# Kernel optimization log

Hardware: AMD Instinct MI355X
Metric: run time of the kernel (lower is better)

The kernel has to match this reference:

```python
import jax, jax.numpy as jnp
import numpy as np

N_HEAD = 16
N_EMBD = 1024
BLOCK = 2048
B, T = 4, 2048


def setup_inputs() -> dict:
    key = jax.random.key(0)
    ks = jax.random.split(key, 5)
    scale = 1.0 / np.sqrt(N_EMBD)
    return {
        "x": jax.random.normal(ks[0], (B, T, N_EMBD), dtype=jnp.float32),
        "W_attn": jax.random.normal(ks[1], (N_EMBD, 3 * N_EMBD), dtype=jnp.float32) * scale,
        "b_attn": jax.random.normal(ks[2], (3 * N_EMBD,), dtype=jnp.float32) * 0.02,
        "W_proj": jax.random.normal(ks[3], (N_EMBD, N_EMBD), dtype=jnp.float32) * scale,
        "b_proj": jax.random.normal(ks[4], (N_EMBD,), dtype=jnp.float32) * 0.02,
    }


def reference(x, W_attn, b_attn, W_proj, b_proj):
    Bb, Tt, C = x.shape
    hd = C // N_HEAD
    qkv = x @ W_attn + b_attn                      # [B,T,3C]
    q, k, v = jnp.split(qkv, 3, axis=2)
    # [B,H,T,hd]
    q = q.reshape(Bb, Tt, N_HEAD, hd).transpose(0, 2, 1, 3)
    k = k.reshape(Bb, Tt, N_HEAD, hd).transpose(0, 2, 1, 3)
    v = v.reshape(Bb, Tt, N_HEAD, hd).transpose(0, 2, 1, 3)
    att = jnp.einsum('bhqd,bhkd->bhqk', q, k) / np.sqrt(hd).astype(x.dtype)
    causal = jnp.tril(jnp.ones((Tt, Tt), dtype=bool))
    att = jnp.where(causal[None, None], att, jnp.finfo(att.dtype).min)
    att = jax.nn.softmax(att, axis=-1)
    y = jnp.einsum('bhqk,bhkd->bhqd', att, v)      # [B,H,T,hd]
    y = y.transpose(0, 2, 1, 3).reshape(Bb, Tt, C)
    return y @ W_proj + b_proj
```

## Files before the change

kernel.cpp:

```cpp
#include <hip/hip_runtime.h>
#include <stdint.h>

typedef unsigned short u16;
typedef __bf16 bf16;
typedef bf16 bf16x8 __attribute__((ext_vector_type(8)));
typedef float f32x4 __attribute__((ext_vector_type(4)));
typedef u16 u16x8 __attribute__((ext_vector_type(8)));
typedef u16 u16x4 __attribute__((ext_vector_type(4)));

#define T_SEQ 2048
#define NHEAD 16
#define HD    64
#define CEMB  1024
#define QS    8388608
#define QSCALE 0.18033688011112042f

__device__ __forceinline__ u16 f2b(float f){
  bf16 h = (bf16)f;
  return __builtin_bit_cast(u16, h);
}
__device__ __forceinline__ void glds16(const void* g, const void* l){
  __builtin_amdgcn_global_load_lds(
    (__attribute__((address_space(1))) unsigned int*)(uintptr_t)g,
    (__attribute__((address_space(3))) unsigned int*)(uintptr_t)l,
    16, 0, 0);
}

__global__ __launch_bounds__(256) void conv_f32_bf16(
    const float* __restrict__ src, u16* __restrict__ dst)
{
  const int i = (blockIdx.x * 256 + threadIdx.x) * 8;
  f32x4 a = *(const f32x4*)&src[i];
  f32x4 b = *(const f32x4*)&src[i + 4];
  u16x8 h;
  #pragma unroll
  for (int j = 0; j < 4; j++){ h[j] = f2b(a[j]); h[4+j] = f2b(b[j]); }
  *(u16x8*)&dst[i] = h;
}

__global__ __launch_bounds__(256) void transpose_f32_bf16(
    const float* __restrict__ src, u16* __restrict__ dst, int K, int N)
{
  __shared__ __align__(16) u16 tile[64][72];
  const int n0 = blockIdx.x * 64, k0 = blockIdx.y * 64;
  const int tid = threadIdx.x;
  #pragma unroll
  for (int it = 0; it < 4; it++){
    const int idx = it * 256 + tid;
    const int row = idx >> 4, c4 = (idx & 15) * 4;
    f32x4 v = *(const f32x4*)&src[(size_t)(k0 + row) * N + n0 + c4];
    #pragma unroll
    for (int j = 0; j < 4; j++) tile[row][c4 + j] = f2b(v[j]);
  }
  __syncthreads();
  const int r = tid >> 3, cc = (tid & 7) * 8;
  #pragma unroll
  for (int i = 0; i < 2; i++){
    const int rr = r + i * 32;
    u16x8 v;
    #pragma unroll
    for (int j = 0; j < 8; j++) v[j] = tile[cc + j][rr];
    *(u16x8*)&dst[(size_t)(n0 + rr) * K + k0 + cc] = v;
  }
}

template<int MODE>
__global__ __launch_bounds__(256) void gemm_bt(
    const u16* __restrict__ A, const u16* __restrict__ Bt,
    const float* __restrict__ bias, void* __restrict__ outraw, int Ktot)
{
  __shared__ __align__(16) u16 As[128*64];
  __shared__ __align__(16) u16 Bs[128*64];
  const int tid = threadIdx.x;
  const int lane = tid & 63, wave = tid >> 6;
  const int l15 = lane & 15, l4 = lane >> 4;
  const int wm = wave >> 1, wn = wave & 1;
  const int m0 = blockIdx.y * 128, n0 = blockIdx.x * 128;

  f32x4 acc[4][4] = {};

  for (int k0 = 0; k0 < Ktot; k0 += 64){
    #pragma unroll
    for (int ii = 0; ii < 4; ii++){
      const int slot0 = (wave*4 + ii) * 64;
      const int s = slot0 + lane;
      const int row = s >> 3;
      const int c = (s & 7) ^ (row & 7);
      glds16(&A [(size_t)(m0 + row) * Ktot + k0 + c*8], &As[slot0*8]);
      glds16(&Bt[(size_t)(n0 + row) * Ktot + k0 + c*8], &Bs[slot0*8]);
    }
    __syncthreads();
    #pragma unroll
    for (int ks = 0; ks < 2; ks++){
      bf16x8 af[4], bfr[4];
      #pragma unroll
      for (int mt = 0; mt < 4; mt++){
        const int rf = wm*64 + mt*16 + l15;
        const int slot = rf*8 + ((ks*4 + l4) ^ (rf & 7));
        af[mt] = *(const bf16x8*)&As[slot*8];
      }
      #pragma unroll
      for (int nt = 0; nt < 4; nt++){
        const int rf = wn*64 + nt*16 + l15;
        const int slot = rf*8 + ((ks*4 + l4) ^ (rf & 7));
        bfr[nt] = *(const bf16x8*)&Bs[slot*8];
      }
      #pragma unroll
      for (int mt = 0; mt < 4; mt++)
        #pragma unroll
        for (int nt = 0; nt < 4; nt++)
          acc[mt][nt] = __builtin_amdgcn_mfma_f32_16x16x32_bf16(
              af[mt], bfr[nt], acc[mt][nt], 0, 0, 0);
    }
    __syncthreads();
  }

  #pragma unroll
  for (int nt = 0; nt < 4; nt++){
    const int n = n0 + wn*64 + nt*16 + l15;
    const float bias_v = bias[n];
    if (MODE == 0){
      u16* out = (u16*)outraw;
      const int which = n >> 10;
      const int cc = n & 1023;
      const int h = cc >> 6, d = cc & 63;
      const float sc = (which == 0) ? QSCALE : 1.0f;
      if (which == 2){
        #pragma unroll
        for (int mt = 0; mt < 4; mt++){
          const int rowg = m0 + wm*64 + mt*16 + l4*4;
          const int bb = rowg >> 11, t = rowg & 2047;
          u16x4 pk;
          #pragma unroll
          for (int r = 0; r < 4; r++) pk[r] = f2b(acc[mt][nt][r] + bias_v);
          *(u16x4*)&out[(size_t)2*QS + ((size_t)(bb*NHEAD + h)*HD + d)*T_SEQ + t] = pk;
        }
      } else {
        #pragma unroll
        for (int mt = 0; mt < 4; mt++)
          #pragma unroll
          for (int r = 0; r < 4; r++){
            const int rowg = m0 + wm*64 + mt*16 + l4*4 + r;
            const int bb = rowg >> 11, t = rowg & 2047;
            out[(size_t)which*QS + ((size_t)(bb*NHEAD + h)*T_SEQ + t)*HD + d]
                = f2b((acc[mt][nt][r] + bias_v) * sc);
          }
      }
    } else {
      float* out = (float*)outraw;
      #pragma unroll
      for (int mt = 0; mt < 4; mt++)
        #pragma unroll
        for (int r = 0; r < 4; r++){
          const int rowg = m0 + wm*64 + mt*16 + l4*4 + r;
          out[(size_t)rowg*CEMB + n] = acc[mt][nt][r] + bias_v;
        }
    }
  }
}

__global__ __launch_bounds__(256) void attn_kernel(
    const u16* __restrict__ qb, const u16* __restrict__ kb,
    const u16* __restrict__ vtb, u16* __restrict__ y)
{
  __shared__ __align__(16) u16 Ks[64*72];
  __shared__ __align__(16) u16 Vt[64*72];
  __shared__ __align__(16) u16 Pw[4*16*72];
  const int tid = threadIdx.x;
  const int lane = tid & 63, wave = tid >> 6;
  const int l15 = lane & 15, l4 = lane >> 4;
  const int qt = 31 - (blockIdx.x >> 6);
  const int bh = blockIdx.x & 63;
  const int q0 = qt * 64;
  const size_t base = (size_t)bh * (T_SEQ * HD);
  const u16* qp  = qb  + base;
  const u16* kp  = kb  + base;
  const u16* vtp = vtb + base;

  const int qg = q0 + wave*16 + l15;

  bf16x8 qf[2];
  {
    const int m = q0 + wave*16 + l15;
    qf[0] = *(const bf16x8*)&qp[m*HD +      l4*8];
    qf[1] = *(const bf16x8*)&qp[m*HD + 32 + l4*8];
  }
  f32x4 o[4] = {};
  float l_run = 0.0f;

  const int prow = tid >> 3, pch = tid & 7;
  const int prow2 = (tid + 256) >> 3, pch2 = tid & 7;
  u16x8 kr0, kr1, vr0, vr1;
  kr0 = *(const u16x8*)&kp [prow *HD + pch *8];
  kr1 = *(const u16x8*)&kp [prow2*HD + pch2*8];
  vr0 = *(const u16x8*)&vtp[(size_t)prow *T_SEQ + pch *8];
  vr1 = *(const u16x8*)&vtp[(size_t)prow2*T_SEQ + pch2*8];

  for (int kt = 0; kt <= qt; kt++){
    __syncthreads();
    *(u16x8*)&Ks[prow *72 + pch *8] = kr0;
    *(u16x8*)&Ks[prow2*72 + pch2*8] = kr1;
    *(u16x8*)&Vt[prow *72 + pch *8] = vr0;
    *(u16x8*)&Vt[prow2*72 + pch2*8] = vr1;
    if (kt < qt){
      kr0 = *(const u16x8*)&kp [(kt+1)*4096 + prow *HD + pch *8];
      kr1 = *(const u16x8*)&kp [(kt+1)*4096 + prow2*HD + pch2*8];
      vr0 = *(const u16x8*)&vtp[(size_t)prow *T_SEQ + (kt+1)*64 + pch *8];
      vr1 = *(const u16x8*)&vtp[(size_t)prow2*T_SEQ + (kt+1)*64 + pch2*8];
    }
    __syncthreads();

    f32x4 sfr[4];
    #pragma unroll
    for (int nb = 0; nb < 4; nb++){
      f32x4 a = {};
      #pragma unroll
      for (int ks = 0; ks < 2; ks++){
        bf16x8 kf = *(const bf16x8*)&Ks[(nb*16 + l15)*72 + ks*32 + l4*8];
        a = __builtin_amdgcn_mfma_f32_16x16x32_bf16(kf, qf[ks], a, 0, 0, 0);
      }
      sfr[nb] = a;
    }

    float pv[4][4];
    if (kt == qt){
      #pragma unroll
      for (int nb = 0; nb < 4; nb++)
        #pragma unroll
        for (int r = 0; r < 4; r++){
          const int t = kt*64 + nb*16 + l4*4 + r;
          float p = __builtin_amdgcn_exp2f(sfr[nb][r]);
          p = (t <= qg) ? p : 0.0f;
          pv[nb][r] = p;
          l_run += p;
        }
    } else {
      #pragma unroll
      for (int nb = 0; nb < 4; nb++)
        #pragma unroll
        for (int r = 0; r < 4; r++){
          const float p = __builtin_amdgcn_exp2f(sfr[nb][r]);
          pv[nb][r] = p;
          l_run += p;
        }
    }

    #pragma unroll
    for (int nb = 0; nb < 4; nb++){
      u16x4 pk;
      #pragma unroll
      for (int r = 0; r < 4; r++) pk[r] = f2b(pv[nb][r]);
      *(u16x4*)&Pw[wave*1152 + l15*72 + nb*16 + l4*4] = pk;
    }

    #pragma unroll
    for (int ks = 0; ks < 2; ks++){
      bf16x8 pf = *(const bf16x8*)&Pw[wave*1152 + l15*72 + ks*32 + l4*8];
      #pragma unroll
      for (int nh = 0; nh < 4; nh++){
        bf16x8 vf = *(const bf16x8*)&Vt[(nh*16 + l15)*72 + ks*32 + l4*8];
        o[nh] = __builtin_amdgcn_mfma_f32_16x16x32_bf16(vf, pf, o[nh], 0, 0, 0);
      }
    }
  }

  l_run += __shfl_xor(l_run, 16);
  l_run += __shfl_xor(l_run, 32);

  const int b = bh >> 4, h = bh & 15;
  const float inv_l = 1.0f / l_run;
  const int t = q0 + wave*16 + l15;
  #pragma unroll
  for (int nh = 0; nh < 4; nh++){
    u16x4 pk;
    #pragma unroll
    for (int r = 0; r < 4; r++) pk[r] = f2b(o[nh][r] * inv_l);
    *(u16x4*)&y[((size_t)(b*T_SEQ + t))*CEMB + h*HD + nh*16 + l4*4] = pk;
  }
}

extern "C" void kernel_launch(void* const* d_in, const int* in_sizes, int n_in,
                              void* d_out, int out_size, void* d_ws, size_t ws_size,
                              hipStream_t stream) {
  const float* x      = (const float*)d_in[0];
  const float* W_attn = (const float*)d_in[1];
  const float* b_attn = (const float*)d_in[2];
  const float* W_proj = (const float*)d_in[3];
  const float* b_proj = (const float*)d_in[4];
  float* out = (float*)d_out;
  u16* ws  = (u16*)d_ws;

  u16* Wt_attn = ws;
  u16* Wt_proj = ws + 3145728;
  u16* xb      = ws + 4194304;
  u16* qkv     = ws + 12582912;
  u16* y       = xb;

  conv_f32_bf16<<<4096, 256, 0, stream>>>(x, xb);
  transpose_f32_bf16<<<dim3(48, 16), 256, 0, stream>>>(W_attn, Wt_attn, 1024, 3072);
  transpose_f32_bf16<<<dim3(16, 16), 256, 0, stream>>>(W_proj, Wt_proj, 1024, 1024);
  gemm_bt<0><<<dim3(24, 64), 256, 0, stream>>>(xb, Wt_attn, b_attn, qkv, 1024);
  attn_kernel<<<2048, 256, 0, stream>>>(qkv, qkv + QS, qkv + 2*QS, y);
  gemm_bt<1><<<dim3(8, 64), 256, 0, stream>>>(y, Wt_proj, b_proj, out, 1024);
}
```

Measured before the change: 257.8 us.

## Enlarge attention query tile, load K/V directly to LDS, fuse prep kernels

The attention kernel now handles 128 queries per block, with each wave owning two 16-row query groups. Each K/V tile loaded into LDS therefore feeds twice as many queries, and the grid is halved. K and V^T tiles are now copied straight into XOR-swizzled LDS with global_load_lds instead of register staging. This removes the software prefetch, so global latency is no longer overlapped with compute. The three preprocessing kernels (x conversion and two weight transposes) are merged into one launch to cut launch overhead.

```diff
diff --git a/kernel.cpp b/kernel.cpp
--- a/kernel.cpp
+++ b/kernel.cpp
@@ -26,24 +26,28 @@
     16, 0, 0);
 }
 
-__global__ __launch_bounds__(256) void conv_f32_bf16(
-    const float* __restrict__ src, u16* __restrict__ dst)
-{
-  const int i = (blockIdx.x * 256 + threadIdx.x) * 8;
-  f32x4 a = *(const f32x4*)&src[i];
-  f32x4 b = *(const f32x4*)&src[i + 4];
-  u16x8 h;
-  #pragma unroll
-  for (int j = 0; j < 4; j++){ h[j] = f2b(a[j]); h[4+j] = f2b(b[j]); }
-  *(u16x8*)&dst[i] = h;
-}
-
-__global__ __launch_bounds__(256) void transpose_f32_bf16(
-    const float* __restrict__ src, u16* __restrict__ dst, int K, int N)
+__global__ __launch_bounds__(256) void prep_kernel(
+    const float* __restrict__ x, u16* __restrict__ xb,
+    const float* __restrict__ Wa, u16* __restrict__ Wta,
+    const float* __restrict__ Wp, u16* __restrict__ Wtp)
 {
   __shared__ __align__(16) u16 tile[64][72];
-  const int n0 = blockIdx.x * 64, k0 = blockIdx.y * 64;
+  const int bid = blockIdx.x;
   const int tid = threadIdx.x;
+  if (bid < 4096){
+    const int i = (bid * 256 + tid) * 8;
+    f32x4 a = *(const f32x4*)&x[i];
+    f32x4 b = *(const f32x4*)&x[i + 4];
+    u16x8 h;
+    #pragma unroll
+    for (int j = 0; j < 4; j++){ h[j] = f2b(a[j]); h[4+j] = f2b(b[j]); }
+    *(u16x8*)&xb[i] = h;
+    return;
+  }
+  const float* src; u16* dst; int K, N, bx, by;
+  if (bid < 4864){ const int j = bid - 4096; src = Wa; dst = Wta; K = 1024; N = 3072; bx = j % 48; by = j / 48; }
+  else           { const int j = bid - 4864; src = Wp; dst = Wtp; K = 1024; N = 1024; bx = j % 16; by = j / 16; }
+  const int n0 = bx * 64, k0 = by * 64;
   #pragma unroll
   for (int it = 0; it < 4; it++){
     const int idx = it * 256 + tid;
@@ -159,123 +163,144 @@
   }
 }
 
-__global__ __launch_bounds__(256) void attn_kernel(
+__global__ __launch_bounds__(256, 4) void attn_kernel(
     const u16* __restrict__ qb, const u16* __restrict__ kb,
     const u16* __restrict__ vtb, u16* __restrict__ y)
 {
-  __shared__ __align__(16) u16 Ks[64*72];
-  __shared__ __align__(16) u16 Vt[64*72];
-  __shared__ __align__(16) u16 Pw[4*16*72];
+  __shared__ __align__(16) u16 Ks[64*64];
+  __shared__ __align__(16) u16 Vt[64*64];
+  __shared__ __align__(16) u16 Pw[8*16*72];
   const int tid = threadIdx.x;
   const int lane = tid & 63, wave = tid >> 6;
   const int l15 = lane & 15, l4 = lane >> 4;
-  const int qt = 31 - (blockIdx.x >> 6);
+  const int qt = 15 - (blockIdx.x >> 6);
   const int bh = blockIdx.x & 63;
-  const int q0 = qt * 64;
+  const int q0 = qt * 128;
   const size_t base = (size_t)bh * (T_SEQ * HD);
   const u16* qp  = qb  + base;
   const u16* kp  = kb  + base;
   const u16* vtp = vtb + base;
 
-  const int qg = q0 + wave*16 + l15;
-
-  bf16x8 qf[2];
-  {
-    const int m = q0 + wave*16 + l15;
-    qf[0] = *(const bf16x8*)&qp[m*HD +      l4*8];
-    qf[1] = *(const bf16x8*)&qp[m*HD + 32 + l4*8];
-  }
-  f32x4 o[4] = {};
-  float l_run = 0.0f;
-
-  const int prow = tid >> 3, pch = tid & 7;
-  const int prow2 = (tid + 256) >> 3, pch2 = tid & 7;
-  u16x8 kr0, kr1, vr0, vr1;
-  kr0 = *(const u16x8*)&kp [prow *HD + pch *8];
-  kr1 = *(const u16x8*)&kp [prow2*HD + pch2*8];
-  vr0 = *(const u16x8*)&vtp[(size_t)prow *T_SEQ + pch *8];
-  vr1 = *(const u16x8*)&vtp[(size_t)prow2*T_SEQ + pch2*8];
-
-  for (int kt = 0; kt <= qt; kt++){
+  const int qmin0 = q0 + wave*32;
+  const int qmin1 = qmin0 + 16;
+
+  bf16x8 qf[2][2];
+  #pragma unroll
+  for (int g = 0; g < 2; g++){
+    const int m = qmin0 + g*16 + l15;
+    qf[g][0] = *(const bf16x8*)&qp[m*HD +      l4*8];
+    qf[g][1] = *(const bf16x8*)&qp[m*HD + 32 + l4*8];
+  }
+  f32x4 o[2][4] = {};
+  float l_run[2] = {0.f, 0.f};
+
+  const int s0i = (wave*2 + 0) * 64 + lane;
+  const int s1i = (wave*2 + 1) * 64 + lane;
+  const int row0 = s0i >> 3, c0 = (s0i & 7) ^ (row0 & 7);
+  const int row1 = s1i >> 3, c1 = (s1i & 7) ^ (row1 & 7);
+  const int koff0 = row0*HD + c0*8, koff1 = row1*HD + c1*8;
+  const int voff0 = row0*T_SEQ + c0*8, voff1 = row1*T_SEQ + c1*8;
+  const int ldso0 = (wave*2 + 0) * 64 * 8, ldso1 = (wave*2 + 1) * 64 * 8;
+
+  const int nkt = 2*qt + 2;
+  for (int kt = 0; kt < nkt; kt++){
     __syncthreads();
-    *(u16x8*)&Ks[prow *72 + pch *8] = kr0;
-    *(u16x8*)&Ks[prow2*72 + pch2*8] = kr1;
-    *(u16x8*)&Vt[prow *72 + pch *8] = vr0;
-    *(u16x8*)&Vt[prow2*72 + pch2*8] = vr1;
-    if (kt < qt){
-      kr0 = *(const u16x8*)&kp [(kt+1)*4096 + prow *HD + pch *8];
-      kr1 = *(const u16x8*)&kp [(kt+1)*4096 + prow2*HD + pch2*8];
-      vr0 = *(const u16x8*)&vtp[(size_t)prow *T_SEQ + (kt+1)*64 + pch *8];
-      vr1 = *(const u16x8*)&vtp[(size_t)prow2*T_SEQ + (kt+1)*64 + pch2*8];
-    }
+    glds16(&kp [kt*4096 + koff0], &Ks[ldso0]);
+    glds16(&kp [kt*4096 + koff1], &Ks[ldso1]);
+    glds16(&vtp[kt*64   + voff0], &Vt[ldso0]);
+    glds16(&vtp[kt*64   + voff1], &Vt[ldso1]);
     __syncthreads();
 
-    f32x4 sfr[4];
-    #pragma unroll
-    for (int nb = 0; nb < 4; nb++){
-      f32x4 a = {};
+    const int t0 = kt*64;
+    if (t0 <= qmin1 + 15){
+      const bool act0 = (t0 <= qmin0 + 15);
+
+      f32x4 s0[4], s1[4];
+      #pragma unroll
+      for (int nb = 0; nb < 4; nb++){
+        f32x4 a0 = {}, a1 = {};
+        #pragma unroll
+        for (int ks = 0; ks < 2; ks++){
+          const int rf = nb*16 + l15;
+          const int slot = rf*8 + ((ks*4 + l4) ^ (rf & 7));
+          bf16x8 kf = *(const bf16x8*)&Ks[slot*8];
+          a1 = __builtin_amdgcn_mfma_f32_16x16x32_bf16(kf, qf[1][ks], a1, 0, 0, 0);
+          if (act0)
+            a0 = __builtin_amdgcn_mfma_f32_16x16x32_bf16(kf, qf[0][ks], a0, 0, 0, 0);
+        }
+        s1[nb] = a1; s0[nb] = a0;
+      }
+
+      #pragma unroll
+      for (int g = 0; g < 2; g++){
+        if (g == 0 && !act0) continue;
+        f32x4* sf = (g == 0) ? s0 : s1;
+        const int qmin = (g == 0) ? qmin0 : qmin1;
+        const int qg = qmin + l15;
+        float lsum = 0.f;
+        if (t0 + 63 > qmin){
+          #pragma unroll
+          for (int nb = 0; nb < 4; nb++){
+            u16x4 pk;
+            #pragma unroll
+            for (int r = 0; r < 4; r++){
+              const int t = t0 + nb*16 + l4*4 + r;
+              float p = __builtin_amdgcn_exp2f(sf[nb][r]);
+              p = (t <= qg) ? p : 0.0f;
+              lsum += p;
+              pk[r] = f2b(p);
+            }
+            *(u16x4*)&Pw[(wave*2 + g)*1152 + l15*72 + nb*16 + l4*4] = pk;
+          }
+        } else {
+          #pragma unroll
+          for (int nb = 0; nb < 4; nb++){
+            u16x4 pk;
+            #pragma unroll
+            for (int r = 0; r < 4; r++){
+              const float p = __builtin_amdgcn_exp2f(sf[nb][r]);
+              lsum += p;
+              pk[r] = f2b(p);
+            }
+            *(u16x4*)&Pw[(wave*2 + g)*1152 + l15*72 + nb*16 + l4*4] = pk;
+          }
+        }
+        l_run[g] += lsum;
+      }
+
       #pragma unroll
       for (int ks = 0; ks < 2; ks++){
-        bf16x8 kf = *(const bf16x8*)&Ks[(nb*16 + l15)*72 + ks*32 + l4*8];
-        a = __builtin_amdgcn_mfma_f32_16x16x32_bf16(kf, qf[ks], a, 0, 0, 0);
-      }
-      sfr[nb] = a;
-    }
-
-    float pv[4][4];
-    if (kt == qt){
-      #pragma unroll
-      for (int nb = 0; nb < 4; nb++)
-        #pragma unroll
-        for (int r = 0; r < 4; r++){
-          const int t = kt*64 + nb*16 + l4*4 + r;
-          float p = __builtin_amdgcn_exp2f(sfr[nb][r]);
-          p = (t <= qg) ? p : 0.0f;
-          pv[nb][r] = p;
-          l_run += p;
-        }
-    } else {
-      #pragma unroll
-      for (int nb = 0; nb < 4; nb++)
-        #pragma unroll
-        for (int r = 0; r < 4; r++){
-          const float p = __builtin_amdgcn_exp2f(sfr[nb][r]);
-          pv[nb][r] = p;
-          l_run += p;
-        }
-    }
-
-    #pragma unroll
-    for (int nb = 0; nb < 4; nb++){
+        bf16x8 pf1 = *(const bf16x8*)&Pw[(wave*2 + 1)*1152 + l15*72 + ks*32 + l4*8];
+        bf16x8 pf0;
+        if (act0) pf0 = *(const bf16x8*)&Pw[(wave*2 + 0)*1152 + l15*72 + ks*32 + l4*8];
+        #pragma unroll
+        for (int nh = 0; nh < 4; nh++){
+          const int rf = nh*16 + l15;
+          const int slot = rf*8 + ((ks*4 + l4) ^ (rf & 7));
+          bf16x8 vf = *(const bf16x8*)&Vt[slot*8];
+          o[1][nh] = __builtin_amdgcn_mfma_f32_16x16x32_bf16(vf, pf1, o[1][nh], 0, 0, 0);
+          if (act0)
+            o[0][nh] = __builtin_amdgcn_mfma_f32_16x16x32_bf16(vf, pf0, o[0][nh], 0, 0, 0);
+        }
+      }
+    }
+  }
+
+  const int b = bh >> 4, h = bh & 15;
+  #pragma unroll
+  for (int g = 0; g < 2; g++){
+    float lr = l_run[g];
+    lr += __shfl_xor(lr, 16);
+    lr += __shfl_xor(lr, 32);
+    const float inv_l = 1.0f / lr;
+    const int t = qmin0 + g*16 + l15;
+    #pragma unroll
+    for (int nh = 0; nh < 4; nh++){
       u16x4 pk;
       #pragma unroll
-      for (int r = 0; r < 4; r++) pk[r] = f2b(pv[nb][r]);
-      *(u16x4*)&Pw[wave*1152 + l15*72 + nb*16 + l4*4] = pk;
-    }
-
-    #pragma unroll
-    for (int ks = 0; ks < 2; ks++){
-      bf16x8 pf = *(const bf16x8*)&Pw[wave*1152 + l15*72 + ks*32 + l4*8];
-      #pragma unroll
-      for (int nh = 0; nh < 4; nh++){
-        bf16x8 vf = *(const bf16x8*)&Vt[(nh*16 + l15)*72 + ks*32 + l4*8];
-        o[nh] = __builtin_amdgcn_mfma_f32_16x16x32_bf16(vf, pf, o[nh], 0, 0, 0);
-      }
-    }
-  }
-
-  l_run += __shfl_xor(l_run, 16);
-  l_run += __shfl_xor(l_run, 32);
-
-  const int b = bh >> 4, h = bh & 15;
-  const float inv_l = 1.0f / l_run;
-  const int t = q0 + wave*16 + l15;
-  #pragma unroll
-  for (int nh = 0; nh < 4; nh++){
-    u16x4 pk;
-    #pragma unroll
-    for (int r = 0; r < 4; r++) pk[r] = f2b(o[nh][r] * inv_l);
-    *(u16x4*)&y[((size_t)(b*T_SEQ + t))*CEMB + h*HD + nh*16 + l4*4] = pk;
+      for (int r = 0; r < 4; r++) pk[r] = f2b(o[g][nh][r] * inv_l);
+      *(u16x4*)&y[((size_t)(b*T_SEQ + t))*CEMB + h*HD + nh*16 + l4*4] = pk;
+    }
   }
 }
 
@@ -296,10 +321,8 @@
   u16* qkv     = ws + 12582912;
   u16* y       = xb;
 
-  conv_f32_bf16<<<4096, 256, 0, stream>>>(x, xb);
-  transpose_f32_bf16<<<dim3(48, 16), 256, 0, stream>>>(W_attn, Wt_attn, 1024, 3072);
-  transpose_f32_bf16<<<dim3(16, 16), 256, 0, stream>>>(W_proj, Wt_proj, 1024, 1024);
+  prep_kernel<<<5120, 256, 0, stream>>>(x, xb, W_attn, Wt_attn, W_proj, Wt_proj);
   gemm_bt<0><<<dim3(24, 64), 256, 0, stream>>>(xb, Wt_attn, b_attn, qkv, 1024);
-  attn_kernel<<<2048, 256, 0, stream>>>(qkv, qkv + QS, qkv + 2*QS, y);
+  attn_kernel<<<1024, 256, 0, stream>>>(qkv, qkv + QS, qkv + 2*QS, y);
   gemm_bt<1><<<dim3(8, 64), 256, 0, stream>>>(y, Wt_proj, b_proj, out, 1024);
 }
```

Result: faster. 241.3 us (-6.4%).
